# Performance work log

Hardware: AMD Instinct MI355X
Metric: run time of the kernel (lower is better)

Reference implementation:

```python
import math
import jax, jax.numpy as jnp
import numpy as np

N = 8192
IN_DIM = 512
INTER = 512
HID = 1024
OUT = 512
GROUPS = 16
EPS = 1e-5


def setup_inputs() -> dict:
    key = jax.random.key(0)
    ks = jax.random.split(key, 12)
    w = lambda k, shape: jax.random.normal(k, shape, jnp.float32) * 0.02
    return {
        "h": jax.random.normal(ks[0], (N, IN_DIM), jnp.float32),
        "D": jax.random.uniform(ks[1], (N, N), dtype=jnp.float32),
        "h_prime": jax.random.normal(ks[2], (N, OUT), jnp.float32),
        "Wq": w(ks[3], (INTER, IN_DIM)), "bq": jnp.zeros((INTER,), jnp.float32),
        "Wk": w(ks[4], (INTER, IN_DIM)), "bk": jnp.zeros((INTER,), jnp.float32),
        "Wv": w(ks[5], (INTER, IN_DIM)), "bv": jnp.zeros((INTER,), jnp.float32),
        "Wr": w(ks[6], (HID, INTER)), "br": jnp.zeros((HID,), jnp.float32),
        "Wc": w(ks[7], (HID, OUT)), "bc": jnp.zeros((HID,), jnp.float32),
        "Wp": w(ks[8], (OUT, 2 * HID)), "bp": jnp.zeros((OUT,), jnp.float32),
        "alpha": jnp.full((OUT,), 0.25, jnp.float32),       # PReLU per-channel slope
        "gamma": jnp.ones((OUT,), jnp.float32),             # GroupNorm weight
        "beta": jnp.zeros((OUT,), jnp.float32),             # GroupNorm bias
    }


def reference(h, D, h_prime, Wq, bq, Wk, bk, Wv, bv, Wr, br, Wc, bc, Wp, bp, alpha, gamma, beta):
    Q = h @ Wq.T + bq                                    # [N, inter]
    K = h @ Wk.T + bk
    V = h @ Wv.T + bv
    scores = (Q @ K.T) / math.sqrt(INTER)                # [N, N]
    attn = jax.nn.softmax(D * scores, axis=-1)           # decay-masked softmax
    h_ret = attn @ V                                     # [N, inter]
    h_ret = jax.nn.gelu(h_ret @ Wr.T + br, approximate=False)  # torch GELU (erf)
    h_cat = h_prime @ Wc.T + bc                          # [N, hid]
    x = jnp.concatenate([h_ret, h_cat], axis=-1) @ Wp.T + bp   # [N, out]
    x = jnp.where(x >= 0, x, alpha * x)                  # PReLU, per-channel
    # GroupNorm over [1, out, N]: stats per group over (channels_in_group, N)
    xT = x.T                                             # [out, N]
    grp = xT.reshape(GROUPS, (OUT // GROUPS) * N)
    mean = grp.mean(axis=1, keepdims=True)
    var = grp.var(axis=1, keepdims=True)
    grp = (grp - mean) * jax.lax.rsqrt(var + EPS)
    xT = grp.reshape(OUT, N) * gamma[:, None] + beta[:, None]
    return xT.T                                          # [N, out]
```

## Files before the change

kernel.cpp:

```cpp
#include <hip/hip_runtime.h>
#include <stdint.h>
#include <math.h>

typedef float f32x4 __attribute__((ext_vector_type(4)));
typedef __bf16 bf16x8 __attribute__((ext_vector_type(8)));
typedef unsigned int u32x4 __attribute__((ext_vector_type(4)));
typedef unsigned short u16;

#define DEVINL static __device__ __forceinline__

DEVINL u16 f2bf(float f) {
  union { float f; unsigned u; } x; x.f = f;
  unsigned r = x.u + 0x7fffu + ((x.u >> 16) & 1u);
  return (u16)(r >> 16);
}

DEVINL void gload_lds16(const void* g, void* l) {
  __builtin_amdgcn_global_load_lds(
      (__attribute__((address_space(1))) void*)(g),
      (__attribute__((address_space(3))) void*)(l), 16, 0, 0);
}

__global__ void cast_kernel(const float* __restrict__ src, u16* __restrict__ dst, int n) {
  int i = (blockIdx.x * 256 + threadIdx.x) * 4;
  if (i >= n) return;
  float4 v = *(const float4*)(src + i);
  u16 o[4] = { f2bf(v.x), f2bf(v.y), f2bf(v.z), f2bf(v.w) };
  *(uint64_t*)(dst + i) = *(uint64_t*)o;
}

template<int EPI>
__global__ __launch_bounds__(256, 2) void gemm_nt(
    const u16* __restrict__ A, int lda, const u16* __restrict__ B, int ldb,
    void* __restrict__ C, int ldc, int coff,
    const float* __restrict__ bias, const float* __restrict__ alpha,
    int N128, int K, float scale, int map)
{
  __shared__ __align__(16) u16 at[2][128 * 64];
  __shared__ __align__(16) u16 bt[2][128 * 64];
  const int tid = threadIdx.x;
  const int w = tid >> 6, lane = tid & 63, r = lane & 15, kg = lane >> 4;
  int bm, bn;
  if (map == 1)      { const int x = blockIdx.x & 7, i = blockIdx.x >> 3; bm = x * 8 + (i >> 2); bn = i & 3; }
  else if (map == 2) { const int x = blockIdx.x & 7, i = blockIdx.x >> 3; bm = x * 8 + (i >> 6); bn = i & 63; }
  else               { bm = blockIdx.x / N128; bn = blockIdx.x % N128; }
  const int m0 = bm * 128, n0 = bn * 128;

  f32x4 acc[4][4];
  #pragma unroll
  for (int m = 0; m < 4; ++m)
    #pragma unroll
    for (int n = 0; n < 4; ++n) acc[m][n] = f32x4{0.f, 0.f, 0.f, 0.f};

  const int srow = tid >> 3, sc = tid & 7;
  const int nk = K >> 6;

  #pragma unroll
  for (int i = 0; i < 4; ++i) {
    int row = srow + i * 32, cs = (sc ^ row) & 7;
    gload_lds16(A + (size_t)(m0 + row) * lda + cs * 8, at[0] + i * 2048 + w * 512);
    gload_lds16(B + (size_t)(n0 + row) * ldb + cs * 8, bt[0] + i * 2048 + w * 512);
  }
  __syncthreads();

  for (int kt = 0; kt < nk; ++kt) {
    const int cur = kt & 1;
    if (kt + 1 < nk) {
      #pragma unroll
      for (int i = 0; i < 4; ++i) {
        int row = srow + i * 32, cs = (sc ^ row) & 7;
        int kcol = (kt + 1) * 64 + cs * 8;
        gload_lds16(A + (size_t)(m0 + row) * lda + kcol, at[cur ^ 1] + i * 2048 + w * 512);
        gload_lds16(B + (size_t)(n0 + row) * ldb + kcol, bt[cur ^ 1] + i * 2048 + w * 512);
      }
    }
    #pragma unroll
    for (int ks = 0; ks < 2; ++ks) {
      bf16x8 af[4], bff[4];
      #pragma unroll
      for (int m = 0; m < 4; ++m) {
        int row = (w >> 1) * 64 + m * 16 + r;
        int cs = ((ks * 4 + kg) ^ row) & 7;
        af[m] = *(const bf16x8*)(at[cur] + row * 64 + cs * 8);
      }
      #pragma unroll
      for (int n = 0; n < 4; ++n) {
        int row = (w & 1) * 64 + n * 16 + r;
        int cs = ((ks * 4 + kg) ^ row) & 7;
        bff[n] = *(const bf16x8*)(bt[cur] + row * 64 + cs * 8);
      }
      #pragma unroll
      for (int m = 0; m < 4; ++m)
        #pragma unroll
        for (int n = 0; n < 4; ++n)
          acc[m][n] = __builtin_amdgcn_mfma_f32_16x16x32_bf16(af[m], bff[n], acc[m][n], 0, 0, 0);
    }
    __syncthreads();
  }

  #pragma unroll
  for (int m = 0; m < 4; ++m) {
    #pragma unroll
    for (int n = 0; n < 4; ++n) {
      const int gcol = n0 + (w & 1) * 64 + n * 16 + r;
      #pragma unroll
      for (int reg = 0; reg < 4; ++reg) {
        const int grow = m0 + (w >> 1) * 64 + m * 16 + kg * 4 + reg;
        float v = acc[m][n][reg];
        if (EPI == 0) v = (v + bias[gcol]) * scale;
        if (EPI == 1) v = v + bias[grow];
        if (EPI == 2) { v += bias[gcol]; v = 0.5f * v * (1.f + erff(v * 0.70710678118654752f)); }
        if (EPI == 4) v = v * scale;
        if (EPI == 5) v = v / bias[grow];
        if (EPI == 3) {
          v += bias[gcol];
          float a = alpha[gcol];
          v = (v >= 0.f) ? v : a * v;
          ((float*)C)[(size_t)grow * ldc + coff + gcol] = v;
        } else {
          ((u16*)C)[(size_t)grow * ldc + coff + gcol] = f2bf(v);
        }
      }
    }
  }
}

__global__ __launch_bounds__(256) void exp_kernel(
    u16* __restrict__ SP, const float* __restrict__ Dm, float* __restrict__ ls)
{
  const int w = threadIdx.x >> 6, lane = threadIdx.x & 63;
  const int row = blockIdx.x * 4 + w;
  u16* sp = SP + (size_t)row * 8192;
  const float* dp = Dm + (size_t)row * 8192;
  float acc = 0.f;
  #pragma unroll 2
  for (int it = 0; it < 16; ++it) {
    const int c = it * 512 + lane * 8;
    const u32x4 sv = *(const u32x4*)(sp + c);
    const u32x4 d0 = __builtin_nontemporal_load((const u32x4*)(dp + c));
    const u32x4 d1 = __builtin_nontemporal_load((const u32x4*)(dp + c + 4));
    u32x4 ow;
    #pragma unroll
    for (int kp = 0; kp < 4; ++kp) {
      union { unsigned u; float f; } s0, s1, e0, e1;
      s0.u = (sv[kp] & 0xffffu) << 16;
      s1.u = sv[kp] & 0xffff0000u;
      e0.u = (kp < 2) ? d0[kp * 2] : d1[(kp - 2) * 2];
      e1.u = (kp < 2) ? d0[kp * 2 + 1] : d1[(kp - 2) * 2 + 1];
      const float p0 = __expf(s0.f * e0.f);
      const float p1 = __expf(s1.f * e1.f);
      acc += p0 + p1;
      ow[kp] = (unsigned)f2bf(p0) | ((unsigned)f2bf(p1) << 16);
    }
    *(u32x4*)(sp + c) = ow;
  }
  #pragma unroll
  for (int m = 1; m < 64; m <<= 1) acc += __shfl_xor(acc, m);
  if (lane == 0) ls[row] = acc;
}

__global__ void gn_stats_kernel(const float* __restrict__ x, float* __restrict__ part) {
  const int g = blockIdx.x >> 4, ch = blockIdx.x & 15;
  const int t = threadIdx.x;
  float s = 0.f, ss = 0.f;
  const int cl = (t & 7) * 4;
  const int r0 = ch * 512 + (t >> 3);
  for (int i = 0; i < 16; ++i) {
    const float4 v = *(const float4*)(x + (size_t)(r0 + i * 32) * 512 + g * 32 + cl);
    s += v.x + v.y + v.z + v.w;
    ss += v.x * v.x + v.y * v.y + v.z * v.z + v.w * v.w;
  }
  #pragma unroll
  for (int m = 1; m < 64; m <<= 1) { s += __shfl_xor(s, m); ss += __shfl_xor(ss, m); }
  __shared__ float red[8];
  const int w = t >> 6, lane = t & 63;
  if (lane == 0) { red[w * 2] = s; red[w * 2 + 1] = ss; }
  __syncthreads();
  if (t == 0) {
    part[blockIdx.x * 2]     = red[0] + red[2] + red[4] + red[6];
    part[blockIdx.x * 2 + 1] = red[1] + red[3] + red[5] + red[7];
  }
}

__global__ void gn_finalize_kernel(const float* __restrict__ part, float* __restrict__ mv) {
  const int g = threadIdx.x;
  if (g < 16) {
    float s = 0.f, ss = 0.f;
    for (int ch = 0; ch < 16; ++ch) {
      s  += part[(g * 16 + ch) * 2];
      ss += part[(g * 16 + ch) * 2 + 1];
    }
    const float mean = s * (1.f / 262144.f);
    const float var = ss * (1.f / 262144.f) - mean * mean;
    mv[g * 2] = mean;
    mv[g * 2 + 1] = rsqrtf(var + 1e-5f);
  }
}

__global__ void gn_norm_kernel(const float* __restrict__ x, const float* __restrict__ mv,
                               const float* __restrict__ gamma, const float* __restrict__ beta,
                               float* __restrict__ out) {
  const int idx = (blockIdx.x * 256 + threadIdx.x) * 4;
  const int c = idx & 511, g = c >> 5;
  const float mean = mv[g * 2], rs = mv[g * 2 + 1];
  float4 v = *(const float4*)(x + idx);
  const float4 gm = *(const float4*)(gamma + c);
  const float4 bt = *(const float4*)(beta + c);
  v.x = (v.x - mean) * rs * gm.x + bt.x;
  v.y = (v.y - mean) * rs * gm.y + bt.y;
  v.z = (v.z - mean) * rs * gm.z + bt.z;
  v.w = (v.w - mean) * rs * gm.w + bt.w;
  *(float4*)(out + idx) = v;
}

extern "C" void kernel_launch(void* const* d_in, const int* in_sizes, int n_in,
                              void* d_out, int out_size, void* d_ws, size_t ws_size,
                              hipStream_t stream) {
  (void)in_sizes; (void)n_in; (void)out_size; (void)ws_size;
  const float* h     = (const float*)d_in[0];
  const float* Dm    = (const float*)d_in[1];
  const float* hp    = (const float*)d_in[2];
  const float* Wq    = (const float*)d_in[3];
  const float* bq    = (const float*)d_in[4];
  const float* Wk    = (const float*)d_in[5];
  const float* bk    = (const float*)d_in[6];
  const float* Wv    = (const float*)d_in[7];
  const float* bv    = (const float*)d_in[8];
  const float* Wr    = (const float*)d_in[9];
  const float* br    = (const float*)d_in[10];
  const float* Wc    = (const float*)d_in[11];
  const float* bc    = (const float*)d_in[12];
  const float* Wp    = (const float*)d_in[13];
  const float* bp    = (const float*)d_in[14];
  const float* alpha = (const float*)d_in[15];
  const float* gamma = (const float*)d_in[16];
  const float* beta  = (const float*)d_in[17];

  char* ws = (char*)d_ws;
  const size_t MB = 1ull << 20;
  u16*   S    = (u16*)(ws);
  u16*   hb   = (u16*)(ws);
  u16*   xcat = (u16*)(ws);
  float* xf   = (float*)(ws + 32 * MB);
  u16*   hpb  = (u16*)(ws + 128 * MB);
  u16*   Qb   = (u16*)(ws + 144 * MB);
  u16*   hrb  = (u16*)(ws + 144 * MB);
  u16*   Kb   = (u16*)(ws + 152 * MB);
  u16*   VTb  = (u16*)(ws + 160 * MB);
  u16*   Wqb  = (u16*)(ws + 168 * MB);
  u16*   Wkb  = Wqb + 262144;
  u16*   Wvb  = Wkb + 262144;
  u16*   Wrb  = Wvb + 262144;
  u16*   Wcb  = Wrb + 524288;
  u16*   Wpb  = Wcb + 524288;
  float* lsum = (float*)(ws + 168 * MB + 5767168);
  float* gp   = lsum + 8192;
  float* mv   = gp + 512;

  cast_kernel<<<4096, 256, 0, stream>>>(h, hb, 4194304);
  cast_kernel<<<4096, 256, 0, stream>>>(hp, hpb, 4194304);
  cast_kernel<<<256, 256, 0, stream>>>(Wq, Wqb, 262144);
  cast_kernel<<<256, 256, 0, stream>>>(Wk, Wkb, 262144);
  cast_kernel<<<256, 256, 0, stream>>>(Wv, Wvb, 262144);
  cast_kernel<<<512, 256, 0, stream>>>(Wr, Wrb, 524288);
  cast_kernel<<<512, 256, 0, stream>>>(Wc, Wcb, 524288);
  cast_kernel<<<1024, 256, 0, stream>>>(Wp, Wpb, 1048576);

  gemm_nt<0><<<256, 256, 0, stream>>>(hb, 512, Wqb, 512, Qb, 512, 0, bq, nullptr, 4, 512, 0.044194173824159216f, 0);
  gemm_nt<0><<<256, 256, 0, stream>>>(hb, 512, Wkb, 512, Kb, 512, 0, bk, nullptr, 4, 512, 1.0f, 0);
  gemm_nt<1><<<256, 256, 0, stream>>>(Wvb, 512, hb, 512, VTb, 8192, 0, bv, nullptr, 64, 512, 1.0f, 0);

  gemm_nt<4><<<4096, 256, 0, stream>>>(Qb, 512, Kb, 512, S, 8192, 0, nullptr, nullptr, 64, 512, 1.0f, 2);

  exp_kernel<<<2048, 256, 0, stream>>>(S, Dm, lsum);

  gemm_nt<5><<<256, 256, 0, stream>>>(S, 8192, VTb, 8192, hrb, 512, 0, lsum, nullptr, 4, 8192, 1.0f, 1);

  gemm_nt<2><<<512, 256, 0, stream>>>(hrb, 512, Wrb, 512, xcat, 2048, 0, br, nullptr, 8, 512, 1.0f, 0);
  gemm_nt<0><<<512, 256, 0, stream>>>(hpb, 512, Wcb, 512, xcat, 2048, 1024, bc, nullptr, 8, 512, 1.0f, 0);

  gemm_nt<3><<<256, 256, 0, stream>>>(xcat, 2048, Wpb, 2048, xf, 512, 0, bp, alpha, 4, 2048, 1.0f, 0);

  gn_stats_kernel<<<256, 256, 0, stream>>>(xf, gp);
  gn_finalize_kernel<<<1, 64, 0, stream>>>(gp, mv);
  gn_norm_kernel<<<4096, 256, 0, stream>>>(xf, mv, gamma, beta, (float*)d_out);
}
```

Measured before the change: 462.8 us.

## Fuse decay-masked exp and partial row sums into QK^T GEMM epilogue

Moves the D-multiply and exp from a separate pass into the score GEMM epilogue, writing bf16 probabilities directly and per-block partial row sums. A small rowsum kernel then reduces the partials. This removes one full write and read of the bf16 score matrix. In exchange, D is loaded with scalar, less coalesced accesses in the epilogue, which may raise register pressure and memory inefficiency there.

```diff
diff --git a/kernel.cpp b/kernel.cpp
--- a/kernel.cpp
+++ b/kernel.cpp
@@ -34,7 +34,8 @@
     const u16* __restrict__ A, int lda, const u16* __restrict__ B, int ldb,
     void* __restrict__ C, int ldc, int coff,
     const float* __restrict__ bias, const float* __restrict__ alpha,
-    int N128, int K, float scale, int map)
+    int N128, int K, float scale, int map,
+    const float* __restrict__ Dmat, float* __restrict__ psum)
 {
   __shared__ __align__(16) u16 at[2][128 * 64];
   __shared__ __align__(16) u16 bt[2][128 * 64];
@@ -98,6 +99,36 @@
     __syncthreads();
   }
 
+  if (EPI == 6) {
+    #pragma unroll
+    for (int m = 0; m < 4; ++m) {
+      float rs[4] = {0.f, 0.f, 0.f, 0.f};
+      #pragma unroll
+      for (int n = 0; n < 4; ++n) {
+        const int gcol = n0 + (w & 1) * 64 + n * 16 + r;
+        #pragma unroll
+        for (int reg = 0; reg < 4; ++reg) {
+          const int grow = m0 + (w >> 1) * 64 + m * 16 + kg * 4 + reg;
+          const float dv = __builtin_nontemporal_load(Dmat + (size_t)grow * 8192 + gcol);
+          const float p = __expf(acc[m][n][reg] * dv);
+          rs[reg] += p;
+          ((u16*)C)[(size_t)grow * ldc + gcol] = f2bf(p);
+        }
+      }
+      #pragma unroll
+      for (int reg = 0; reg < 4; ++reg) {
+        float v = rs[reg];
+        v += __shfl_xor(v, 1); v += __shfl_xor(v, 2);
+        v += __shfl_xor(v, 4); v += __shfl_xor(v, 8);
+        if (r == 0) {
+          const int grow = m0 + (w >> 1) * 64 + m * 16 + kg * 4 + reg;
+          psum[(size_t)grow * 128 + bn * 2 + (w & 1)] = v;
+        }
+      }
+    }
+    return;
+  }
+
   #pragma unroll
   for (int m = 0; m < 4; ++m) {
     #pragma unroll
@@ -110,7 +141,6 @@
         if (EPI == 0) v = (v + bias[gcol]) * scale;
         if (EPI == 1) v = v + bias[grow];
         if (EPI == 2) { v += bias[gcol]; v = 0.5f * v * (1.f + erff(v * 0.70710678118654752f)); }
-        if (EPI == 4) v = v * scale;
         if (EPI == 5) v = v / bias[grow];
         if (EPI == 3) {
           v += bias[gcol];
@@ -125,38 +155,15 @@
   }
 }
 
-__global__ __launch_bounds__(256) void exp_kernel(
-    u16* __restrict__ SP, const float* __restrict__ Dm, float* __restrict__ ls)
-{
-  const int w = threadIdx.x >> 6, lane = threadIdx.x & 63;
-  const int row = blockIdx.x * 4 + w;
-  u16* sp = SP + (size_t)row * 8192;
-  const float* dp = Dm + (size_t)row * 8192;
-  float acc = 0.f;
-  #pragma unroll 2
-  for (int it = 0; it < 16; ++it) {
-    const int c = it * 512 + lane * 8;
-    const u32x4 sv = *(const u32x4*)(sp + c);
-    const u32x4 d0 = __builtin_nontemporal_load((const u32x4*)(dp + c));
-    const u32x4 d1 = __builtin_nontemporal_load((const u32x4*)(dp + c + 4));
-    u32x4 ow;
-    #pragma unroll
-    for (int kp = 0; kp < 4; ++kp) {
-      union { unsigned u; float f; } s0, s1, e0, e1;
-      s0.u = (sv[kp] & 0xffffu) << 16;
-      s1.u = sv[kp] & 0xffff0000u;
-      e0.u = (kp < 2) ? d0[kp * 2] : d1[(kp - 2) * 2];
-      e1.u = (kp < 2) ? d0[kp * 2 + 1] : d1[(kp - 2) * 2 + 1];
-      const float p0 = __expf(s0.f * e0.f);
-      const float p1 = __expf(s1.f * e1.f);
-      acc += p0 + p1;
-      ow[kp] = (unsigned)f2bf(p0) | ((unsigned)f2bf(p1) << 16);
-    }
-    *(u32x4*)(sp + c) = ow;
-  }
-  #pragma unroll
-  for (int m = 1; m < 64; m <<= 1) acc += __shfl_xor(acc, m);
-  if (lane == 0) ls[row] = acc;
+__global__ __launch_bounds__(256) void rowsum_kernel(const float* __restrict__ psum,
+                                                     float* __restrict__ ls) {
+  const int row = blockIdx.x * 4 + (threadIdx.x >> 6);
+  const int lane = threadIdx.x & 63;
+  const float2 v = *(const float2*)(psum + (size_t)row * 128 + lane * 2);
+  float s = v.x + v.y;
+  #pragma unroll
+  for (int m = 1; m < 64; m <<= 1) s += __shfl_xor(s, m);
+  if (lane == 0) ls[row] = s;
 }
 
 __global__ void gn_stats_kernel(const float* __restrict__ x, float* __restrict__ part) {
@@ -238,7 +245,7 @@
 
   char* ws = (char*)d_ws;
   const size_t MB = 1ull << 20;
-  u16*   S    = (u16*)(ws);
+  u16*   P    = (u16*)(ws);
   u16*   hb   = (u16*)(ws);
   u16*   xcat = (u16*)(ws);
   float* xf   = (float*)(ws + 32 * MB);
@@ -256,6 +263,7 @@
   float* lsum = (float*)(ws + 168 * MB + 5767168);
   float* gp   = lsum + 8192;
   float* mv   = gp + 512;
+  float* psum = (float*)(ws + 176 * MB);
 
   cast_kernel<<<4096, 256, 0, stream>>>(h, hb, 4194304);
   cast_kernel<<<4096, 256, 0, stream>>>(hp, hpb, 4194304);
@@ -266,20 +274,19 @@
   cast_kernel<<<512, 256, 0, stream>>>(Wc, Wcb, 524288);
   cast_kernel<<<1024, 256, 0, stream>>>(Wp, Wpb, 1048576);
 
-  gemm_nt<0><<<256, 256, 0, stream>>>(hb, 512, Wqb, 512, Qb, 512, 0, bq, nullptr, 4, 512, 0.044194173824159216f, 0);
-  gemm_nt<0><<<256, 256, 0, stream>>>(hb, 512, Wkb, 512, Kb, 512, 0, bk, nullptr, 4, 512, 1.0f, 0);
-  gemm_nt<1><<<256, 256, 0, stream>>>(Wvb, 512, hb, 512, VTb, 8192, 0, bv, nullptr, 64, 512, 1.0f, 0);
-
-  gemm_nt<4><<<4096, 256, 0, stream>>>(Qb, 512, Kb, 512, S, 8192, 0, nullptr, nullptr, 64, 512, 1.0f, 2);
-
-  exp_kernel<<<2048, 256, 0, stream>>>(S, Dm, lsum);
-
-  gemm_nt<5><<<256, 256, 0, stream>>>(S, 8192, VTb, 8192, hrb, 512, 0, lsum, nullptr, 4, 8192, 1.0f, 1);
-
-  gemm_nt<2><<<512, 256, 0, stream>>>(hrb, 512, Wrb, 512, xcat, 2048, 0, br, nullptr, 8, 512, 1.0f, 0);
-  gemm_nt<0><<<512, 256, 0, stream>>>(hpb, 512, Wcb, 512, xcat, 2048, 1024, bc, nullptr, 8, 512, 1.0f, 0);
-
-  gemm_nt<3><<<256, 256, 0, stream>>>(xcat, 2048, Wpb, 2048, xf, 512, 0, bp, alpha, 4, 2048, 1.0f, 0);
+  gemm_nt<0><<<256, 256, 0, stream>>>(hb, 512, Wqb, 512, Qb, 512, 0, bq, nullptr, 4, 512, 0.044194173824159216f, 0, nullptr, nullptr);
+  gemm_nt<0><<<256, 256, 0, stream>>>(hb, 512, Wkb, 512, Kb, 512, 0, bk, nullptr, 4, 512, 1.0f, 0, nullptr, nullptr);
+  gemm_nt<1><<<256, 256, 0, stream>>>(Wvb, 512, hb, 512, VTb, 8192, 0, bv, nullptr, 64, 512, 1.0f, 0, nullptr, nullptr);
+
+  gemm_nt<6><<<4096, 256, 0, stream>>>(Qb, 512, Kb, 512, P, 8192, 0, nullptr, nullptr, 64, 512, 1.0f, 2, Dm, psum);
+  rowsum_kernel<<<2048, 256, 0, stream>>>(psum, lsum);
+
+  gemm_nt<5><<<256, 256, 0, stream>>>(P, 8192, VTb, 8192, hrb, 512, 0, lsum, nullptr, 4, 8192, 1.0f, 1, nullptr, nullptr);
+
+  gemm_nt<2><<<512, 256, 0, stream>>>(hrb, 512, Wrb, 512, xcat, 2048, 0, br, nullptr, 8, 512, 1.0f, 0, nullptr, nullptr);
+  gemm_nt<0><<<512, 256, 0, stream>>>(hpb, 512, Wcb, 512, xcat, 2048, 1024, bc, nullptr, 8, 512, 1.0f, 0, nullptr, nullptr);
+
+  gemm_nt<3><<<256, 256, 0, stream>>>(xcat, 2048, Wpb, 2048, xf, 512, 0, bp, alpha, 4, 2048, 1.0f, 0, nullptr, nullptr);
 
   gn_stats_kernel<<<256, 256, 0, stream>>>(xf, gp);
   gn_finalize_kernel<<<1, 64, 0, stream>>>(gp, mv);
```

Result: faster. 439.3 us (-5.1%).
